# Optimization experiments

Hardware: AMD Instinct MI355X
Metric: run time of the kernel (lower is better)

Reference implementation:

```python
import jax, jax.numpy as jnp
import numpy as np

IN_FEATURES = 4096
OUT_FEATURES = 4096
N_TOKENS = 8192  # flattened batch*seq


def setup_inputs() -> dict:
    key = jax.random.key(0)
    kx, kw = jax.random.split(key)
    x = jax.random.normal(kx, (N_TOKENS, IN_FEATURES), dtype=jnp.float16)
    # Full weight [out, in], split into a 2:4 structured part and the complement
    # (mirrors prune_2_to_4's [0,0,1,1] pattern along the in dim).
    W = jax.random.normal(kw, (OUT_FEATURES, IN_FEATURES), dtype=jnp.float16)
    pattern = jnp.asarray([0, 0, 1, 1], dtype=jnp.float16)
    mask = jnp.tile(pattern, IN_FEATURES // 4)  # [in]
    W_dense = W * mask          # 2:4 semi-structured component
    W_sparse = W * (1 - mask)   # unstructured CSR component (complement)
    return {"x": x, "W_dense": W_dense, "W_sparse": W_sparse}


def reference(x, W_dense, W_sparse):
    # Original: out_dense = W_semi @ x^T ; out_sparse = spmm(W_csr, x^T)
    #           out = out_sparse^T + out_dense^T
    # Equivalent: x @ W_dense^T + x @ W_sparse^T, two separate GEMMs summed.
    out_dense = jnp.einsum('ni,oi->no', x, W_dense)
    out_sparse = jnp.einsum('ni,oi->no', x, W_sparse)
    return out_dense + out_sparse
```

## Files before the change

kernel.cpp:

```cpp
#include <hip/hip_runtime.h>
#include <stdint.h>


#define NT 8192
#define NO 4096
#define NK 4096

typedef float f32x4 __attribute__((ext_vector_type(4)));
typedef _Float16 f16x8 __attribute__((ext_vector_type(8)));

__device__ __forceinline__ void gload_lds16(const void* g, void* l) {
  __builtin_amdgcn_global_load_lds(
      (const __attribute__((address_space(1))) void*)g,
      (__attribute__((address_space(3))) void*)l, 16, 0, 0);
}

#define BAR() __builtin_amdgcn_s_barrier()
#define WV6() asm volatile("s_waitcnt vmcnt(6)" ::: "memory")
#define PRIO1() __builtin_amdgcn_s_setprio(1)
#define PRIO0() __builtin_amdgcn_s_setprio(0)


__global__ __launch_bounds__(256) void cvt_x_kernel(
    const float* __restrict__ x, _Float16* __restrict__ o, int n8) {
  int i = blockIdx.x * 256 + threadIdx.x;
  if (i >= n8) return;
  const f32x4* p = (const f32x4*)x + 2 * (size_t)i;
  f32x4 lo = p[0], hi = p[1];
  f16x8 r;
#pragma unroll
  for (int j = 0; j < 4; ++j) { r[j] = (_Float16)lo[j]; r[j + 4] = (_Float16)hi[j]; }
  *((f16x8*)o + i) = r;
}

__global__ __launch_bounds__(256) void cvt_w_kernel(
    const float* __restrict__ wd, const float* __restrict__ ws,
    _Float16* __restrict__ o, int n8) {
  int i = blockIdx.x * 256 + threadIdx.x;
  if (i >= n8) return;
  const f32x4* pd = (const f32x4*)wd + 2 * (size_t)i;
  const f32x4* ps = (const f32x4*)ws + 2 * (size_t)i;
  f32x4 dl = pd[0], dh = pd[1], sl = ps[0], sh = ps[1];
  f16x8 r;
#pragma unroll
  for (int j = 0; j < 4; ++j) {
    r[j] = (_Float16)(dl[j] + sl[j]);
    r[j + 4] = (_Float16)(dh[j] + sh[j]);
  }
  *((f16x8*)o + i) = r;
}


#define RDA(B_, MG) do { _Pragma("unroll") \
  for (int mm = 0; mm < 4; ++mm) { \
    ar[0][mm] = *(const f16x8*)(Ab[B_] + ((MG)*8 + mm*2 + 0) * 1024 + finner); \
    ar[1][mm] = *(const f16x8*)(Ab[B_] + ((MG)*8 + mm*2 + 1) * 1024 + finner); \
  } } while (0)

#define RDB(B_, NG) do { _Pragma("unroll") \
  for (int nn = 0; nn < 2; ++nn) { \
    br[0][(NG)*2+nn] = *(const f16x8*)(Bb[B_] + ((bsub + (NG)*2 + nn)*2 + 0) * 1024 + finner); \
    br[1][(NG)*2+nn] = *(const f16x8*)(Bb[B_] + ((bsub + (NG)*2 + nn)*2 + 1) * 1024 + finner); \
  } } while (0)

#define MM(MG, NG) do { _Pragma("unroll") \
  for (int ks = 0; ks < 2; ++ks) \
    _Pragma("unroll") for (int mm = 0; mm < 4; ++mm) \
      _Pragma("unroll") for (int nn = 0; nn < 2; ++nn) \
        acc[(MG)*4+mm][(NG)*2+nn] = __builtin_amdgcn_mfma_f32_16x16x32_f16( \
            ar[ks][mm], br[ks][(NG)*2+nn], acc[(MG)*4+mm][(NG)*2+nn], 0, 0, 0); \
  } while (0)

#define STG(BUF_, OP_, H_, S_, KCOL) \
  gload_lds16(((OP_) ? Wrow : Xrow) + ((H_)*128 + (S_)*64) * NK + (KCOL), \
              ldsc + (BUF_)*65536 + (OP_)*32768 + (H_)*16384 + (S_)*8192 + t16)

__global__ __launch_bounds__(512, 2) void gemm8p(
    const _Float16* __restrict__ Xg, const _Float16* __restrict__ Wg,
    float* __restrict__ C) {
  __shared__ _Float16 lds[2][2][2][8192];
  char* ldsc = (char*)&lds[0][0][0][0];

  const int t = threadIdx.x;
  const int lane = t & 63;
  const int wv = t >> 6;
  const int wr = wv >> 2;
  const int wc = wv & 3;
  const int fr = lane & 15;
  const int kq = lane >> 4;
  const int t16 = t * 16;

  const int swz = (blockIdx.x & 7) * 64 + (blockIdx.x >> 3);
  const int bm = swz >> 4, bn = swz & 15;
  const int brow = bm * 256, bcol = bn * 256;

  const int o = t16;
  const int sub = o >> 10;
  const int inner = o & 1023;
  const int innsw = inner ^ (((inner >> 9) & 1) << 5);
  const int rloc = ((sub >> 1) << 4) | ((innsw >> 6) & 15);
  const int kloc = ((sub & 1) << 5) | ((innsw >> 1) & 31);

  const _Float16* Xrow = Xg + (brow + rloc) * NK + kloc;
  const _Float16* Wrow = Wg + (bcol + rloc) * NK + kloc;

  const int finner = ((fr << 6) | (kq << 4)) ^ ((fr & 8) << 2);
  const char* Ab[2] = { ldsc + wr * 16384, ldsc + 65536 + wr * 16384 };
  const char* Bb[2] = { ldsc + 32768 + (wc >> 1) * 16384,
                        ldsc + 65536 + 32768 + (wc >> 1) * 16384 };
  const int bsub = (wc & 1) * 4;

  f16x8 ar[2][4], br[2][4];
  f32x4 acc[8][4] = {};

  STG(0, 0, 0, 0, 0); STG(0, 0, 0, 1, 0); STG(0, 0, 1, 0, 0); STG(0, 0, 1, 1, 0);
  STG(0, 1, 0, 0, 0); STG(0, 1, 0, 1, 0); STG(0, 1, 1, 0, 0); STG(0, 1, 1, 1, 0);
  STG(1, 0, 0, 0, 64); STG(1, 0, 1, 0, 64);
  STG(1, 1, 0, 0, 64); STG(1, 1, 0, 1, 64); STG(1, 1, 1, 0, 64); STG(1, 1, 1, 1, 64);
  WV6(); BAR();

#pragma unroll 1
  for (int i = 0; i < NK / 128; ++i) {
    const int k1 = i * 128 + 64;
    const int kt2 = (i * 128 + 128) & (NK - 1);
    const int kt3 = (i * 128 + 192) & (NK - 1);

    RDA(0, 0); RDB(0, 0);
    STG(1, 0, 0, 1, k1); STG(1, 0, 1, 1, k1);
    PRIO1(); MM(0, 0); PRIO0(); BAR();
    RDB(0, 1);
    STG(0, 0, 0, 0, kt2); STG(0, 0, 1, 0, kt2);
    PRIO1(); MM(0, 1); PRIO0(); BAR();
    RDA(0, 1);
    STG(0, 1, 0, 0, kt2); STG(0, 1, 0, 1, kt2);
    PRIO1(); MM(1, 0); PRIO0(); BAR();
    STG(0, 1, 1, 0, kt2); STG(0, 1, 1, 1, kt2);
    PRIO1(); MM(1, 1); PRIO0();
    WV6(); BAR();
    RDA(1, 0); RDB(1, 0);
    STG(0, 0, 0, 1, kt2); STG(0, 0, 1, 1, kt2);
    PRIO1(); MM(0, 0); PRIO0(); BAR();
    RDB(1, 1);
    STG(1, 0, 0, 0, kt3); STG(1, 0, 1, 0, kt3);
    PRIO1(); MM(0, 1); PRIO0(); BAR();
    RDA(1, 1);
    STG(1, 1, 0, 0, kt3); STG(1, 1, 0, 1, kt3);
    PRIO1(); MM(1, 0); PRIO0(); BAR();
    STG(1, 1, 1, 0, kt3); STG(1, 1, 1, 1, kt3);
    PRIO1(); MM(1, 1); PRIO0();
    WV6(); BAR();
  }

  const int r0 = brow + wr * 128 + kq * 4;
  const int c0 = bcol + wc * 64 + fr;
#pragma unroll
  for (int m = 0; m < 8; ++m)
#pragma unroll
    for (int n = 0; n < 4; ++n)
#pragma unroll
      for (int j = 0; j < 4; ++j)
        C[(r0 + m * 16 + j) * NO + c0 + n * 16] = acc[m][n][j];
}

__global__ __launch_bounds__(256) void gemm_fb(
    const float* __restrict__ Xf, const float* __restrict__ Wdf,
    const float* __restrict__ Wsf, float* __restrict__ C) {
  __shared__ _Float16 lsA[128 * 32];
  __shared__ _Float16 lsB[128 * 32];

  const int t = threadIdx.x;
  const int lane = t & 63;
  const int wid = t >> 6;
  const int wr = wid >> 1, wc = wid & 1;

  const int nwg = (NT / 128) * (NO / 128);
  const int swz = (blockIdx.x & 7) * (nwg >> 3) + (blockIdx.x >> 3);
  const int nbn = NO / 128;
  const int bm = swz / nbn, bn = swz % nbn;
  const long brow = (long)bm * 128, bcol = (long)bn * 128;

  const int srow = t >> 2;
  const int scol = (t & 3) * 8;
  const float* X  = Xf + (brow + srow) * (long)NK + scol;
  const float* Wd = Wdf + (bcol + srow) * (long)NK + scol;
  const float* Ws = Wsf + (bcol + srow) * (long)NK + scol;
  _Float16* lA = lsA + t * 8;
  _Float16* lB = lsB + t * 8;

  const int fr = lane & 15;
  const int kg = (lane >> 4) * 8;
  const _Float16* pA = lsA + (wr * 64 + fr) * 32 + kg;
  const _Float16* pB = lsB + (wc * 64 + fr) * 32 + kg;

  f32x4 acc[4][4] = {};

  for (int k0 = 0; k0 < NK; k0 += 32) {
    f32x4 aL0 = *(const f32x4*)(X + k0),  aH0 = *(const f32x4*)(X + k0 + 4);
    f32x4 aL1 = *(const f32x4*)(X + k0 + 64 * NK), aH1 = *(const f32x4*)(X + k0 + 64 * NK + 4);
    f32x4 dL0 = *(const f32x4*)(Wd + k0), dH0 = *(const f32x4*)(Wd + k0 + 4);
    f32x4 sL0 = *(const f32x4*)(Ws + k0), sH0 = *(const f32x4*)(Ws + k0 + 4);
    f32x4 dL1 = *(const f32x4*)(Wd + k0 + 64 * NK), dH1 = *(const f32x4*)(Wd + k0 + 64 * NK + 4);
    f32x4 sL1 = *(const f32x4*)(Ws + k0 + 64 * NK), sH1 = *(const f32x4*)(Ws + k0 + 64 * NK + 4);
    __syncthreads();
    f16x8 va0, va1, vb0, vb1;
#pragma unroll
    for (int j = 0; j < 4; ++j) {
      va0[j] = (_Float16)aL0[j];            va0[j + 4] = (_Float16)aH0[j];
      va1[j] = (_Float16)aL1[j];            va1[j + 4] = (_Float16)aH1[j];
      vb0[j] = (_Float16)(dL0[j] + sL0[j]); vb0[j + 4] = (_Float16)(dH0[j] + sH0[j]);
      vb1[j] = (_Float16)(dL1[j] + sL1[j]); vb1[j + 4] = (_Float16)(dH1[j] + sH1[j]);
    }
    *(f16x8*)lA = va0;
    *(f16x8*)(lA + 64 * 32) = va1;
    *(f16x8*)lB = vb0;
    *(f16x8*)(lB + 64 * 32) = vb1;
    __syncthreads();
    f16x8 af[4], bf[4];
#pragma unroll
    for (int i2 = 0; i2 < 4; ++i2) af[i2] = *(const f16x8*)(pA + i2 * 16 * 32);
#pragma unroll
    for (int i2 = 0; i2 < 4; ++i2) bf[i2] = *(const f16x8*)(pB + i2 * 16 * 32);
#pragma unroll
    for (int i2 = 0; i2 < 4; ++i2)
#pragma unroll
      for (int j2 = 0; j2 < 4; ++j2)
        acc[i2][j2] = __builtin_amdgcn_mfma_f32_16x16x32_f16(af[i2], bf[j2], acc[i2][j2], 0, 0, 0);
  }

  const int fq = lane >> 4;
#pragma unroll
  for (int i2 = 0; i2 < 4; ++i2)
#pragma unroll
    for (int j2 = 0; j2 < 4; ++j2)
#pragma unroll
      for (int r = 0; r < 4; ++r) {
        long row = brow + wr * 64 + i2 * 16 + fq * 4 + r;
        long col = bcol + wc * 64 + j2 * 16 + fr;
        C[row * NO + col] = acc[i2][j2][r];
      }
}

extern "C" void kernel_launch(void* const* d_in, const int* in_sizes, int n_in,
                              void* d_out, int out_size, void* d_ws, size_t ws_size,
                              hipStream_t stream) {
  const float* x   = (const float*)d_in[0];
  const float* wd  = (const float*)d_in[1];
  const float* wsp = (const float*)d_in[2];
  float* out = (float*)d_out;

  const size_t xh_bytes = (size_t)NT * NK * 2;
  const size_t wh_bytes = (size_t)NO * NK * 2;

  if (d_ws != nullptr && ws_size >= xh_bytes + wh_bytes) {
    _Float16* xh = (_Float16*)d_ws;
    _Float16* wh = (_Float16*)((char*)d_ws + xh_bytes);
    const int nx8 = NT * NK / 8;
    const int nw8 = NO * NK / 8;
    cvt_x_kernel<<<nx8 / 256, 256, 0, stream>>>(x, xh, nx8);
    cvt_w_kernel<<<nw8 / 256, 256, 0, stream>>>(wd, wsp, wh, nw8);
    gemm8p<<<(NT / 256) * (NO / 256), 512, 0, stream>>>(xh, wh, out);
  } else {
    gemm_fb<<<(NT / 128) * (NO / 128), 256, 0, stream>>>(x, wd, wsp, out);
  }
}
```

Before: 298.9 us.

## Merge conversion kernels, transpose MFMA operands for vector stores, reorder LDS reads

The two fp32-to-fp16 conversion kernels become one launch covering both x and the summed weights, which saves a kernel launch and the gap between launches. The MFMA operands are swapped so each lane's four accumulator values are contiguous along the output columns. That lets the epilogue write one 16-byte vector per fragment instead of four scalar strided stores. LDS reads for the second B group are also moved earlier, and a barrier now comes after the next A read, which raises register pressure and changes how loads overlap with compute.

```diff
diff --git a/kernel.cpp b/kernel.cpp
--- a/kernel.cpp
+++ b/kernel.cpp
@@ -20,34 +20,33 @@
 #define PRIO1() __builtin_amdgcn_s_setprio(1)
 #define PRIO0() __builtin_amdgcn_s_setprio(0)
 
-
-__global__ __launch_bounds__(256) void cvt_x_kernel(
-    const float* __restrict__ x, _Float16* __restrict__ o, int n8) {
+__global__ __launch_bounds__(256) void cvt_all(
+    const float* __restrict__ x, const float* __restrict__ wd,
+    const float* __restrict__ ws, _Float16* __restrict__ xh,
+    _Float16* __restrict__ wh, int nx8, int nw8) {
   int i = blockIdx.x * 256 + threadIdx.x;
-  if (i >= n8) return;
-  const f32x4* p = (const f32x4*)x + 2 * (size_t)i;
-  f32x4 lo = p[0], hi = p[1];
-  f16x8 r;
-#pragma unroll
-  for (int j = 0; j < 4; ++j) { r[j] = (_Float16)lo[j]; r[j + 4] = (_Float16)hi[j]; }
-  *((f16x8*)o + i) = r;
-}
-
-__global__ __launch_bounds__(256) void cvt_w_kernel(
-    const float* __restrict__ wd, const float* __restrict__ ws,
-    _Float16* __restrict__ o, int n8) {
-  int i = blockIdx.x * 256 + threadIdx.x;
-  if (i >= n8) return;
-  const f32x4* pd = (const f32x4*)wd + 2 * (size_t)i;
-  const f32x4* ps = (const f32x4*)ws + 2 * (size_t)i;
-  f32x4 dl = pd[0], dh = pd[1], sl = ps[0], sh = ps[1];
-  f16x8 r;
-#pragma unroll
-  for (int j = 0; j < 4; ++j) {
-    r[j] = (_Float16)(dl[j] + sl[j]);
-    r[j + 4] = (_Float16)(dh[j] + sh[j]);
-  }
-  *((f16x8*)o + i) = r;
+  if (i < nx8) {
+    const f32x4* p = (const f32x4*)x + 2 * (size_t)i;
+    f32x4 lo = p[0], hi = p[1];
+    f16x8 r;
+#pragma unroll
+    for (int j = 0; j < 4; ++j) { r[j] = (_Float16)lo[j]; r[j + 4] = (_Float16)hi[j]; }
+    *((f16x8*)xh + i) = r;
+  } else {
+    int j8 = i - nx8;
+    if (j8 < nw8) {
+      const f32x4* pd = (const f32x4*)wd + 2 * (size_t)j8;
+      const f32x4* ps = (const f32x4*)ws + 2 * (size_t)j8;
+      f32x4 dl = pd[0], dh = pd[1], sl = ps[0], sh = ps[1];
+      f16x8 r;
+#pragma unroll
+      for (int j = 0; j < 4; ++j) {
+        r[j] = (_Float16)(dl[j] + sl[j]);
+        r[j + 4] = (_Float16)(dh[j] + sh[j]);
+      }
+      *((f16x8*)wh + j8) = r;
+    }
+  }
 }
 
 
@@ -68,7 +67,7 @@
     _Pragma("unroll") for (int mm = 0; mm < 4; ++mm) \
       _Pragma("unroll") for (int nn = 0; nn < 2; ++nn) \
         acc[(MG)*4+mm][(NG)*2+nn] = __builtin_amdgcn_mfma_f32_16x16x32_f16( \
-            ar[ks][mm], br[ks][(NG)*2+nn], acc[(MG)*4+mm][(NG)*2+nn], 0, 0, 0); \
+            br[ks][(NG)*2+nn], ar[ks][mm], acc[(MG)*4+mm][(NG)*2+nn], 0, 0, 0); \
   } while (0)
 
 #define STG(BUF_, OP_, H_, S_, KCOL) \
@@ -125,41 +124,42 @@
     const int kt2 = (i * 128 + 128) & (NK - 1);
     const int kt3 = (i * 128 + 192) & (NK - 1);
 
-    RDA(0, 0); RDB(0, 0);
+    RDA(0, 0); RDB(0, 0); RDB(0, 1);
     STG(1, 0, 0, 1, k1); STG(1, 0, 1, 1, k1);
     PRIO1(); MM(0, 0); PRIO0(); BAR();
-    RDB(0, 1);
     STG(0, 0, 0, 0, kt2); STG(0, 0, 1, 0, kt2);
-    PRIO1(); MM(0, 1); PRIO0(); BAR();
+    PRIO1(); MM(0, 1); PRIO0();
     RDA(0, 1);
+    BAR();
     STG(0, 1, 0, 0, kt2); STG(0, 1, 0, 1, kt2);
     PRIO1(); MM(1, 0); PRIO0(); BAR();
     STG(0, 1, 1, 0, kt2); STG(0, 1, 1, 1, kt2);
     PRIO1(); MM(1, 1); PRIO0();
     WV6(); BAR();
-    RDA(1, 0); RDB(1, 0);
+    RDA(1, 0); RDB(1, 0); RDB(1, 1);
     STG(0, 0, 0, 1, kt2); STG(0, 0, 1, 1, kt2);
     PRIO1(); MM(0, 0); PRIO0(); BAR();
-    RDB(1, 1);
+
     STG(1, 0, 0, 0, kt3); STG(1, 0, 1, 0, kt3);
-    PRIO1(); MM(0, 1); PRIO0(); BAR();
+    PRIO1(); MM(0, 1); PRIO0();
     RDA(1, 1);
+    BAR();
+
     STG(1, 1, 0, 0, kt3); STG(1, 1, 0, 1, kt3);
     PRIO1(); MM(1, 0); PRIO0(); BAR();
+
     STG(1, 1, 1, 0, kt3); STG(1, 1, 1, 1, kt3);
     PRIO1(); MM(1, 1); PRIO0();
     WV6(); BAR();
   }
 
-  const int r0 = brow + wr * 128 + kq * 4;
-  const int c0 = bcol + wc * 64 + fr;
+  const long r0 = brow + wr * 128 + fr;
+  const int c0 = bcol + wc * 64 + kq * 4;
 #pragma unroll
   for (int m = 0; m < 8; ++m)
 #pragma unroll
     for (int n = 0; n < 4; ++n)
-#pragma unroll
-      for (int j = 0; j < 4; ++j)
-        C[(r0 + m * 16 + j) * NO + c0 + n * 16] = acc[m][n][j];
+      *(f32x4*)(C + (r0 + m * 16) * NO + c0 + n * 16) = acc[m][n];
 }
 
 __global__ __launch_bounds__(256) void gemm_fb(
@@ -256,8 +256,7 @@
     _Float16* wh = (_Float16*)((char*)d_ws + xh_bytes);
     const int nx8 = NT * NK / 8;
     const int nw8 = NO * NK / 8;
-    cvt_x_kernel<<<nx8 / 256, 256, 0, stream>>>(x, xh, nx8);
-    cvt_w_kernel<<<nw8 / 256, 256, 0, stream>>>(wd, wsp, wh, nw8);
+    cvt_all<<<(nx8 + nw8) / 256, 256, 0, stream>>>(x, wd, wsp, xh, wh, nx8, nw8);
     gemm8p<<<(NT / 256) * (NO / 256), 512, 0, stream>>>(xh, wh, out);
   } else {
     gemm_fb<<<(NT / 128) * (NO / 128), 256, 0, stream>>>(x, wd, wsp, out);
```

Measured after the change: 296.3 us. About the same (-0.9%).
